# Performance work log

Measured on AMD Instinct MI355X. Metric: run time of the kernel, lower is better.

## Reference

```python
import jax, jax.numpy as jnp
import numpy as np

B, T, H, K, C, U, IN = 128, 800, 512, 10, 80, 64, 3


def setup_inputs() -> dict:
    key = jax.random.key(0)
    ks = jax.random.split(key, 6)
    s = 0.08  # small init so exp() window params stay stable
    return {
        "strokes": jax.random.normal(ks[0], (B, T, IN), jnp.float32),
        "sentences": jax.random.randint(ks[1], (B, U), 0, C),
        "sentences_mask": jnp.ones((B, U), jnp.float32),
        "W_ih": jax.random.normal(ks[2], (4 * H, IN + C), jnp.float32) * s,
        "W_hh": jax.random.normal(ks[3], (4 * H, H), jnp.float32) * s,
        "b_ih": jnp.zeros((4 * H,), jnp.float32),
        "b_hh": jnp.zeros((4 * H,), jnp.float32),
        "W_win": jax.random.normal(ks[4], (3 * K, H), jnp.float32) * s,
        "b_win": jnp.zeros((3 * K,), jnp.float32),
    }


def reference(strokes, sentences, sentences_mask, W_ih, W_hh, b_ih, b_hh, W_win, b_win):
    # Pre-mask the one-hot character encoding: [B, U, C]
    onehot = jax.nn.one_hot(sentences, C, dtype=jnp.float32) * sentences_mask[:, :, None]
    u = jnp.arange(U, dtype=jnp.float32)  # character position grid
    bias = b_ih + b_hh

    def step(carry, x_t):
        h, c, kappa_prev, window = carry
        inp = jnp.concatenate([x_t, window], axis=-1)           # [B, IN+C]
        gates = inp @ W_ih.T + h @ W_hh.T + bias                 # [B, 4H]
        i, f, g, o = jnp.split(gates, 4, axis=-1)                # torch LSTMCell order i,f,g,o
        i, f, o = jax.nn.sigmoid(i), jax.nn.sigmoid(f), jax.nn.sigmoid(o)
        c = f * c + i * jnp.tanh(g)
        h = o * jnp.tanh(c)
        # Gaussian window parameters (eq. 48-51 in Graves 2013)
        p = h @ W_win.T + b_win                                  # [B, 3K]
        a_hat, b_hat, k_hat = jnp.split(p, 3, axis=-1)
        alpha = jnp.exp(a_hat)
        beta = jnp.exp(b_hat)
        kappa = kappa_prev + jnp.exp(k_hat)
        # phi[b,u] = sum_k alpha * exp(-beta * (kappa - u)^2)
        d = kappa[:, :, None] - u[None, None, :]                 # [B, K, U]
        phi = jnp.sum(alpha[:, :, None] * jnp.exp(-beta[:, :, None] * d * d), axis=1)  # [B, U]
        window = jnp.einsum('bu,buc->bc', phi, onehot)           # [B, C]
        return (h, c, kappa, window), (h, window, phi)

    init = (
        jnp.zeros((B, H), jnp.float32),
        jnp.zeros((B, H), jnp.float32),
        jnp.zeros((B, K), jnp.float32),
        jnp.zeros((B, C), jnp.float32),
    )
    xs = jnp.swapaxes(strokes, 0, 1)                             # [T, B, IN]
    _, (h_seq, w_seq, phi_seq) = jax.lax.scan(step, init, xs)
    return (
        jnp.swapaxes(h_seq, 0, 1),    # [B, T, H]
        jnp.swapaxes(w_seq, 0, 1),    # [B, T, C]
        jnp.swapaxes(phi_seq, 0, 1),  # [B, T, U]
    )
```

## Files before the change

### kernel.cpp

```cpp
#include <hip/hip_runtime.h>
#include <hip/hip_bf16.h>
#include <math.h>

#define B_   128
#define T_   800
#define H_   512
#define K_   10
#define C_   80
#define U_   64
#define IN_  3
#define SDIM (H_ + C_)

#define NG   4
#define BPG  64
#define BT   32
#define UPB  8
#define RPB  32
#define NT   512

#define WS_ST    0
#define WS_GPP   (2*SDIM*B_)
#define WS_BAR   (WS_GPP + NG*BPG*BT*30)
#define WS_TOTAL (WS_BAR + NG*8*32)

#define OFF_H    0ull
#define OFF_W    ((size_t)B_ * T_ * H_)
#define OFF_PHI  (OFF_W + (size_t)B_ * T_ * C_)

__device__ __forceinline__ void st_bypass(float* p, float v) {
  asm volatile("global_store_dword %0, %1, off sc0 sc1" :: "v"(p), "v"(v) : "memory");
}
__device__ __forceinline__ void fence_vm() {
  asm volatile("s_waitcnt vmcnt(0)" ::: "memory");
}
__device__ __forceinline__ void flag_add(unsigned* p) {
  __hip_atomic_fetch_add(p, 1u, __ATOMIC_RELAXED, __HIP_MEMORY_SCOPE_AGENT);
}
__device__ __forceinline__ unsigned flag_sum(unsigned* base, int nlines) {
  unsigned s = 0;
  for (int i = 0; i < nlines; ++i)
    s += __hip_atomic_load(base + i * 32, __ATOMIC_RELAXED, __HIP_MEMORY_SCOPE_AGENT);
  return s;
}
__device__ __forceinline__ void acq_fence(unsigned* p) {
  (void)__hip_atomic_load(p, __ATOMIC_ACQUIRE, __HIP_MEMORY_SCOPE_AGENT);
}
__device__ __forceinline__ float sigmoidf_(float v) { return 1.0f / (1.0f + expf(-v)); }

__global__ void __launch_bounds__(256, 2)
init_ws_kernel(float* __restrict__ ws) {
  size_t i = (size_t)blockIdx.x * 256 + threadIdx.x;
  const size_t n = (size_t)WS_TOTAL;
  const size_t stride = (size_t)gridDim.x * 256;
  for (; i < n; i += stride) ws[i] = 0.0f;
}

__global__ void __launch_bounds__(NT, 1)
graves_kernel(const float* __restrict__ x,
              const int*   __restrict__ sent,
              const float* __restrict__ smask,
              const float* __restrict__ W_ih,
              const float* __restrict__ W_hh,
              const float* __restrict__ b_ih,
              const float* __restrict__ b_hh,
              const float* __restrict__ W_win,
              const float* __restrict__ b_win,
              float* __restrict__ out,
              float* __restrict__ ws)
{
  const int tid = threadIdx.x;
  const int bid = blockIdx.x;
  const int g   = bid / BPG;
  const int ub  = bid - g * BPG;
  const int b0  = g * BT;
  const int u0  = ub * UPB;

  float* sT  = ws + WS_ST;
  float* gpp = ws + WS_GPP;
  unsigned* fb = (unsigned*)(ws + WS_BAR) + (size_t)g * (8 * 32);
  unsigned* c1 = fb;
  unsigned* c2 = fb + 4 * 32;

  __shared__ __align__(16) float wlds[SDIM][RPB];
  __shared__ float red[NT][17];
  __shared__ float gl[RPB][BT];
  __shared__ float hT[UPB][BT];
  __shared__ float cpl[UPB][BT];
  __shared__ float wwin[UPB][30];
  __shared__ float xwb[RPB][4];
  __shared__ float ppst[BPG][30];
  __shared__ float pl[30];
  __shared__ float abk[3][K_];
  __shared__ float kapl[K_];
  __shared__ float phim[U_];
  __shared__ float phir[U_];
  __shared__ float wl[C_];
  __shared__ int   sentl[U_];
  __shared__ float maskl[U_];

  for (int idx = tid; idx < SDIM * RPB; idx += NT) {
    const int k = idx >> 5, r = idx & 31;
    const int uu = r >> 2, gate = r & 3;
    const int gr = gate * H_ + u0 + uu;
    wlds[k][r] = (k < H_) ? W_hh[(size_t)gr * H_ + k]
                          : W_ih[(size_t)gr * (IN_ + C_) + IN_ + (k - H_)];
  }
  if (tid < RPB) {
    const int uu = tid >> 2, gate = tid & 3, gr = gate * H_ + u0 + uu;
    xwb[tid][0] = W_ih[(size_t)gr * (IN_ + C_) + 0];
    xwb[tid][1] = W_ih[(size_t)gr * (IN_ + C_) + 1];
    xwb[tid][2] = W_ih[(size_t)gr * (IN_ + C_) + 2];
    xwb[tid][3] = b_ih[gr] + b_hh[gr];
  }
  if (tid < UPB * 30) {
    const int uu = tid / 30, j = tid % 30;
    wwin[uu][j] = W_win[(size_t)j * H_ + u0 + uu];
  }
  if (tid < UPB * BT) {
    cpl[tid >> 5][tid & 31] = 0.0f;
  }
  const bool isWB = (ub < BT);
  const int  wb_b = b0 + ub;
  if (isWB) {
    if (tid < U_) {
      sentl[tid] = sent[wb_b * U_ + tid];
      maskl[tid] = smask[wb_b * U_ + tid];
    }
    if (tid < K_) kapl[tid] = 0.0f;
  }
  __syncthreads();

  const int rt  = tid & 7;
  const int bt  = (tid >> 3) & 7;
  const int ks  = tid >> 6;
  const int myb = b0 + 4 * bt;

  for (int t = 0; t < T_; ++t) {
    const int p = t & 1;
    const float* sIn = sT + (size_t)p * (SDIM * B_);
    float*      sOut = sT + (size_t)(1 - p) * (SDIM * B_);

    float acc[4][4];
    #pragma unroll
    for (int i = 0; i < 4; ++i)
      #pragma unroll
      for (int j = 0; j < 4; ++j) acc[i][j] = 0.0f;

    {
      const float* sp = sIn + myb;
      const int k0 = ks * (H_ / 8);
      #pragma unroll 4
      for (int k = k0; k < k0 + H_ / 8; ++k) {
        const float4 s4 = *(const float4*)(sp + (size_t)k * B_);
        const float4 w4 = *(const float4*)(&wlds[k][4 * rt]);
        const float sv[4] = {s4.x, s4.y, s4.z, s4.w};
        const float wv[4] = {w4.x, w4.y, w4.z, w4.w};
        #pragma unroll
        for (int i = 0; i < 4; ++i)
          #pragma unroll
          for (int j = 0; j < 4; ++j) acc[i][j] = fmaf(wv[i], sv[j], acc[i][j]);
      }
    }

    if (tid == 0 && t > 0) {
      const unsigned tgt = (unsigned)(BT * t);
      while (flag_sum(c2, 2) < tgt) __builtin_amdgcn_s_sleep(1);
      acq_fence(c2);
    }
    __syncthreads();

    {
      const float* sp = sIn + myb;
      const int k0 = H_ + ks * (C_ / 8);
      #pragma unroll
      for (int k = k0; k < k0 + C_ / 8; ++k) {
        const float4 s4 = *(const float4*)(sp + (size_t)k * B_);
        const float4 w4 = *(const float4*)(&wlds[k][4 * rt]);
        const float sv[4] = {s4.x, s4.y, s4.z, s4.w};
        const float wv[4] = {w4.x, w4.y, w4.z, w4.w};
        #pragma unroll
        for (int i = 0; i < 4; ++i)
          #pragma unroll
          for (int j = 0; j < 4; ++j) acc[i][j] = fmaf(wv[i], sv[j], acc[i][j]);
      }
    }

    #pragma unroll
    for (int i = 0; i < 4; ++i)
      #pragma unroll
      for (int j = 0; j < 4; ++j) red[tid][i * 4 + j] = acc[i][j];
    __syncthreads();

    for (int it = tid; it < RPB * BT; it += NT) {
      const int r = it >> 5, b = it & 31;
      const int base = (r >> 2) + 8 * (b >> 2);
      const int e = (r & 3) * 4 + (b & 3);
      float v = xwb[r][3];
      #pragma unroll
      for (int kq = 0; kq < 8; ++kq) v += red[base + 64 * kq][e];
      const float* xp = x + ((size_t)(b0 + b) * T_ + t) * IN_;
      v = fmaf(xwb[r][0], xp[0], v);
      v = fmaf(xwb[r][1], xp[1], v);
      v = fmaf(xwb[r][2], xp[2], v);
      gl[r][b] = v;
    }
    __syncthreads();

    if (tid < BT * UPB) {
      const int b = tid & 31, uu = tid >> 5;
      const float iv = sigmoidf_(gl[uu * 4 + 0][b]);
      const float fv = sigmoidf_(gl[uu * 4 + 1][b]);
      const float gv = tanhf(gl[uu * 4 + 2][b]);
      const float ov = sigmoidf_(gl[uu * 4 + 3][b]);
      const float cv = fmaf(fv, cpl[uu][b], iv * gv);
      cpl[uu][b] = cv;
      const float hv = ov * tanhf(cv);
      hT[uu][b] = hv;
      st_bypass(&sOut[(size_t)(u0 + uu) * B_ + b0 + b], hv);
    }
    __syncthreads();

    for (int it = tid; it < BT * 30; it += NT) {
      const int b = it / 30, j = it % 30;
      float s = 0.0f;
      #pragma unroll
      for (int uu = 0; uu < UPB; ++uu) s = fmaf(wwin[uu][j], hT[uu][b], s);
      st_bypass(&gpp[((size_t)(g * BPG + ub) * BT + b) * 30 + j], s);
    }
    fence_vm();
    __syncthreads();
    if (tid == 0) flag_add(c1 + (ub & 3) * 32);

    if (!isWB) {
      if (tid < 64) {
        const int b = tid >> 1, half = tid & 1;
        float4 hv4 = make_float4(hT[half * 4 + 0][b], hT[half * 4 + 1][b],
                                 hT[half * 4 + 2][b], hT[half * 4 + 3][b]);
        *(float4*)&out[OFF_H + ((size_t)(b0 + b) * T_ + t) * H_ + u0 + half * 4] = hv4;
      }
      if (tid == 0) {
        const unsigned tgt = (unsigned)(BPG * (t + 1));
        while (flag_sum(c1, 4) < tgt) __builtin_amdgcn_s_sleep(1);
        acq_fence(c1);
      }
      __syncthreads();
    } else {
      if (tid == 0) {
        const unsigned tgt = (unsigned)(BPG * (t + 1));
        while (flag_sum(c1, 4) < tgt) __builtin_amdgcn_s_sleep(1);
        acq_fence(c1);
      }
      __syncthreads();
      for (int it = tid; it < BPG * 30; it += NT) {
        const int blk = it / 30, j = it % 30;
        ppst[blk][j] = gpp[((size_t)(g * BPG + blk) * BT + ub) * 30 + j];
      }
      __syncthreads();
      if (tid < 30) {
        float s = b_win[tid];
        #pragma unroll
        for (int blk = 0; blk < BPG; ++blk) s += ppst[blk][tid];
        pl[tid] = s;
      }
      __syncthreads();
      if (tid < K_) {
        abk[0][tid] = expf(pl[tid]);
        abk[1][tid] = expf(pl[K_ + tid]);
        const float kv = kapl[tid] + expf(pl[2 * K_ + tid]);
        kapl[tid] = kv;
        abk[2][tid] = kv;
      }
      __syncthreads();
      if (tid < U_) {
        const float fu = (float)tid;
        float s = 0.0f;
        #pragma unroll
        for (int j2 = 0; j2 < K_; ++j2) {
          const float d = abk[2][j2] - fu;
          s = fmaf(abk[0][j2], expf(-abk[1][j2] * d * d), s);
        }
        phim[tid] = s * maskl[tid];
        phir[tid] = s;
      }
      __syncthreads();
      if (tid < C_) {
        float wv = 0.0f;
        #pragma unroll
        for (int u = 0; u < U_; ++u) wv += (sentl[u] == tid) ? phim[u] : 0.0f;
        st_bypass(&sOut[(size_t)(H_ + tid) * B_ + wb_b], wv);
        wl[tid] = wv;
      }
      fence_vm();
      __syncthreads();
      if (tid == 0) flag_add(c2 + (ub & 1) * 32);

      if (tid < 64) {
        const int b = tid >> 1, half = tid & 1;
        float4 hv4 = make_float4(hT[half * 4 + 0][b], hT[half * 4 + 1][b],
                                 hT[half * 4 + 2][b], hT[half * 4 + 3][b]);
        *(float4*)&out[OFF_H + ((size_t)(b0 + b) * T_ + t) * H_ + u0 + half * 4] = hv4;
      }
      if (tid < U_) out[OFF_PHI + ((size_t)wb_b * T_ + t) * U_ + tid] = phir[tid];
      if (tid < C_) out[OFF_W + ((size_t)wb_b * T_ + t) * C_ + tid] = wl[tid];
    }
  }
}

extern "C" void kernel_launch(void* const* d_in, const int* in_sizes, int n_in,
                              void* d_out, int out_size, void* d_ws, size_t ws_size,
                              hipStream_t stream) {
  const float* x     = (const float*)d_in[0];
  const int*   sent  = (const int*)  d_in[1];
  const float* smask = (const float*)d_in[2];
  const float* W_ih  = (const float*)d_in[3];
  const float* W_hh  = (const float*)d_in[4];
  const float* b_ih  = (const float*)d_in[5];
  const float* b_hh  = (const float*)d_in[6];
  const float* W_win = (const float*)d_in[7];
  const float* b_win = (const float*)d_in[8];
  float* ws = (float*)d_ws;
  float* out = (float*)d_out;

  hipLaunchKernelGGL(init_ws_kernel, dim3(512), dim3(256), 0, stream, ws);
  hipLaunchKernelGGL(graves_kernel, dim3(NG * BPG), dim3(NT), 0, stream,
                     x, sent, smask, W_ih, W_hh, b_ih, b_hh, W_win, b_win, out, ws);
}
```

Measured before the change: 11.35 ms.

## Use split-bf16 MFMA for LSTM gate matmul and restructure step pipeline

Replaces the scalar FP32 FMA gate matmul with bf16 MFMA 16x16x32. Weights and state are split into hi and lo bf16 parts and combined over three MFMAs to keep near-FP32 accuracy. State is exchanged as packed hi/lo words in a row-major swizzled LDS layout, and threads per block drop to 256. The window computation is moved to the start of the next step so it can overlap with the h-part of the matmul. This cuts ALU cost, but adds per-step unpacking and changes the synchronisation ordering, and the split-bf16 approximation carries some precision risk.

After: 10.54 ms. 1.08x faster.

```diff
diff --git a/kernel.cpp b/kernel.cpp
--- a/kernel.cpp
+++ b/kernel.cpp
@@ -9,25 +9,32 @@
 #define C_   80
 #define U_   64
 #define IN_  3
-#define SDIM (H_ + C_)
 
 #define NG   4
 #define BPG  64
 #define BT   32
-#define UPB  8
-#define RPB  32
-#define NT   512
-
-#define WS_ST    0
-#define WS_GPP   (2*SDIM*B_)
-#define WS_BAR   (WS_GPP + NG*BPG*BT*30)
-#define WS_TOTAL (WS_BAR + NG*8*32)
+#define NT   256
+#define KROW 608
+
+#define WS_GPP_F (2*B_*KROW)
+#define WS_BAR_F (WS_GPP_F + NG*BPG*BT*30)
+#define WS_TOTAL_F (WS_BAR_F + NG*8*32)
 
 #define OFF_H    0ull
 #define OFF_W    ((size_t)B_ * T_ * H_)
 #define OFF_PHI  (OFF_W + (size_t)B_ * T_ * C_)
 
-__device__ __forceinline__ void st_bypass(float* p, float v) {
+typedef __attribute__((ext_vector_type(8))) short short8;
+typedef __attribute__((ext_vector_type(4))) float f32x4;
+
+#define SWZB(row)    (((row) ^ ((row) >> 2)) & 3)
+#define SWIDX(row,k) ((row)*KROW + ((((k) >> 3) ^ SWZB(row)) << 3) + ((k) & 7))
+#define LDFRAG(arr,row,u) (*(const short8*)&(arr)[(row)*KROW + (((u) ^ SWZB(row)) << 3)])
+
+__device__ __forceinline__ void stb_f32(float* p, float v) {
+  asm volatile("global_store_dword %0, %1, off sc0 sc1" :: "v"(p), "v"(v) : "memory");
+}
+__device__ __forceinline__ void stb_u32(unsigned* p, unsigned v) {
   asm volatile("global_store_dword %0, %1, off sc0 sc1" :: "v"(p), "v"(v) : "memory");
 }
 __device__ __forceinline__ void fence_vm() {
@@ -46,11 +53,17 @@
   (void)__hip_atomic_load(p, __ATOMIC_ACQUIRE, __HIP_MEMORY_SCOPE_AGENT);
 }
 __device__ __forceinline__ float sigmoidf_(float v) { return 1.0f / (1.0f + expf(-v)); }
+__device__ __forceinline__ unsigned pack_hl(float v) {
+  unsigned hb = __float_as_uint(v) >> 16;
+  float rs = v - __uint_as_float(hb << 16);
+  unsigned lb = __float_as_uint(rs) >> 16;
+  return (hb << 16) | lb;
+}
 
 __global__ void __launch_bounds__(256, 2)
 init_ws_kernel(float* __restrict__ ws) {
   size_t i = (size_t)blockIdx.x * 256 + threadIdx.x;
-  const size_t n = (size_t)WS_TOTAL;
+  const size_t n = (size_t)WS_TOTAL_F;
   const size_t stride = (size_t)gridDim.x * 256;
   for (; i < n; i += stride) ws[i] = 0.0f;
 }
@@ -70,205 +83,160 @@
 {
   const int tid = threadIdx.x;
   const int bid = blockIdx.x;
-  const int g   = bid / BPG;
-  const int ub  = bid - g * BPG;
+  const int g   = bid >> 6;
+  const int ub  = bid & (BPG - 1);
   const int b0  = g * BT;
-  const int u0  = ub * UPB;
-
-  float* sT  = ws + WS_ST;
-  float* gpp = ws + WS_GPP;
-  unsigned* fb = (unsigned*)(ws + WS_BAR) + (size_t)g * (8 * 32);
-  unsigned* c1 = fb;
-  unsigned* c2 = fb + 4 * 32;
-
-  __shared__ __align__(16) float wlds[SDIM][RPB];
-  __shared__ float red[NT][17];
-  __shared__ float gl[RPB][BT];
-  __shared__ float hT[UPB][BT];
-  __shared__ float cpl[UPB][BT];
-  __shared__ float wwin[UPB][30];
-  __shared__ float xwb[RPB][4];
-  __shared__ float ppst[BPG][30];
-  __shared__ float pl[30];
-  __shared__ float abk[3][K_];
-  __shared__ float kapl[K_];
-  __shared__ float phim[U_];
-  __shared__ float phir[U_];
-  __shared__ float wl[C_];
+  const int u0  = ub * 8;
+
+  unsigned* gbufu = (unsigned*)ws;
+  float*    gpp   = ws + WS_GPP_F;
+  unsigned* fb    = (unsigned*)(ws + WS_BAR_F) + (size_t)g * 256;
+  unsigned* c1l   = fb;
+  unsigned* c2l   = fb + 4 * 32;
+
+  __shared__ __align__(16) short whi[32 * KROW];
+  __shared__ __align__(16) short wlo[32 * KROW];
+  __shared__ __align__(16) short shi[32 * KROW];
+  __shared__ __align__(16) short slo[32 * KROW];
+  __shared__ __align__(16) float glf[1024];
+  __shared__ float hT[8 * 32];
+  __shared__ float wwin[8 * 30];
+  __shared__ float xwb[32 * 4];
   __shared__ int   sentl[U_];
   __shared__ float maskl[U_];
-
-  for (int idx = tid; idx < SDIM * RPB; idx += NT) {
-    const int k = idx >> 5, r = idx & 31;
-    const int uu = r >> 2, gate = r & 3;
-    const int gr = gate * H_ + u0 + uu;
-    wlds[k][r] = (k < H_) ? W_hh[(size_t)gr * H_ + k]
-                          : W_ih[(size_t)gr * (IN_ + C_) + IN_ + (k - H_)];
-  }
-  if (tid < RPB) {
+  __shared__ float kapl[K_ + 6];
+
+  float* pred  = glf;
+  float* pl    = glf + 256;
+  float* abkA  = glf + 288;
+  float* abkB  = glf + 304;
+  float* abkK  = glf + 320;
+  float* phim  = glf + 336;
+
+  for (int idx = tid; idx < 32 * KROW; idx += NT) {
+    const int r = idx / KROW, k = idx - r * KROW;
+    const int uu = r >> 2, gate = r & 3, gr = gate * H_ + u0 + uu;
+    float wv = 0.0f;
+    if (k < H_)      wv = W_hh[(size_t)gr * H_ + k];
+    else if (k < H_ + C_) wv = W_ih[(size_t)gr * (IN_ + C_) + IN_ + (k - H_)];
+    const unsigned hb = __float_as_uint(wv) >> 16;
+    const float rs = wv - __uint_as_float(hb << 16);
+    const unsigned lb = __float_as_uint(rs) >> 16;
+    const int li = SWIDX(r, k);
+    whi[li] = (short)hb;
+    wlo[li] = (short)lb;
+  }
+  for (int idx = tid; idx < 32 * 16; idx += NT) {
+    const int b2 = idx >> 4, k = (H_ + C_) + (idx & 15);
+    shi[SWIDX(b2, k)] = 0; slo[SWIDX(b2, k)] = 0;
+  }
+  if (tid < 32) {
     const int uu = tid >> 2, gate = tid & 3, gr = gate * H_ + u0 + uu;
-    xwb[tid][0] = W_ih[(size_t)gr * (IN_ + C_) + 0];
-    xwb[tid][1] = W_ih[(size_t)gr * (IN_ + C_) + 1];
-    xwb[tid][2] = W_ih[(size_t)gr * (IN_ + C_) + 2];
-    xwb[tid][3] = b_ih[gr] + b_hh[gr];
-  }
-  if (tid < UPB * 30) {
-    const int uu = tid / 30, j = tid % 30;
-    wwin[uu][j] = W_win[(size_t)j * H_ + u0 + uu];
-  }
-  if (tid < UPB * BT) {
-    cpl[tid >> 5][tid & 31] = 0.0f;
+    xwb[tid * 4 + 0] = W_ih[(size_t)gr * (IN_ + C_) + 0];
+    xwb[tid * 4 + 1] = W_ih[(size_t)gr * (IN_ + C_) + 1];
+    xwb[tid * 4 + 2] = W_ih[(size_t)gr * (IN_ + C_) + 2];
+    xwb[tid * 4 + 3] = b_ih[gr] + b_hh[gr];
+  }
+  for (int idx = tid; idx < 240; idx += NT) {
+    const int uu = idx / 30, j = idx - uu * 30;
+    wwin[idx] = W_win[(size_t)j * H_ + u0 + uu];
   }
   const bool isWB = (ub < BT);
   const int  wb_b = b0 + ub;
   if (isWB) {
-    if (tid < U_) {
-      sentl[tid] = sent[wb_b * U_ + tid];
-      maskl[tid] = smask[wb_b * U_ + tid];
-    }
+    if (tid < U_) { sentl[tid] = sent[wb_b * U_ + tid]; maskl[tid] = smask[wb_b * U_ + tid]; }
     if (tid < K_) kapl[tid] = 0.0f;
   }
   __syncthreads();
 
-  const int rt  = tid & 7;
-  const int bt  = (tid >> 3) & 7;
-  const int ks  = tid >> 6;
-  const int myb = b0 + 4 * bt;
-
-  for (int t = 0; t < T_; ++t) {
-    const int p = t & 1;
-    const float* sIn = sT + (size_t)p * (SDIM * B_);
-    float*      sOut = sT + (size_t)(1 - p) * (SDIM * B_);
-
-    float acc[4][4];
-    #pragma unroll
-    for (int i = 0; i < 4; ++i)
-      #pragma unroll
-      for (int j = 0; j < 4; ++j) acc[i][j] = 0.0f;
-
-    {
-      const float* sp = sIn + myb;
-      const int k0 = ks * (H_ / 8);
-      #pragma unroll 4
-      for (int k = k0; k < k0 + H_ / 8; ++k) {
-        const float4 s4 = *(const float4*)(sp + (size_t)k * B_);
-        const float4 w4 = *(const float4*)(&wlds[k][4 * rt]);
-        const float sv[4] = {s4.x, s4.y, s4.z, s4.w};
-        const float wv[4] = {w4.x, w4.y, w4.z, w4.w};
-        #pragma unroll
-        for (int i = 0; i < 4; ++i)
-          #pragma unroll
-          for (int j = 0; j < 4; ++j) acc[i][j] = fmaf(wv[i], sv[j], acc[i][j]);
-      }
-    }
+  const int lane = tid & 63;
+  const int wid  = tid >> 6;
+  const int ni   = wid & 1;
+  const int kh   = wid >> 1;
+  const int r16  = lane & 15;
+  const int g4   = lane >> 4;
+  const int bb   = ni * 16 + r16;
+
+  float cr0 = 0.0f, cr1 = 0.0f;
+
+#define GSTEP(ks) { \
+    const int uu_ = (ks) * 4 + g4; \
+    const short8 bh = LDFRAG(shi, bb, uu_); \
+    const short8 bl = LDFRAG(slo, bb, uu_); \
+    const short8 ah0 = LDFRAG(whi, r16, uu_); \
+    const short8 al0 = LDFRAG(wlo, r16, uu_); \
+    const short8 ah1 = LDFRAG(whi, 16 + r16, uu_); \
+    const short8 al1 = LDFRAG(wlo, 16 + r16, uu_); \
+    a0 = __builtin_amdgcn_mfma_f32_16x16x32_bf16(ah0, bh, a0, 0, 0, 0); \
+    a0 = __builtin_amdgcn_mfma_f32_16x16x32_bf16(ah0, bl, a0, 0, 0, 0); \
+    a0 = __builtin_amdgcn_mfma_f32_16x16x32_bf16(al0, bh, a0, 0, 0, 0); \
+    a1 = __builtin_amdgcn_mfma_f32_16x16x32_bf16(ah1, bh, a1, 0, 0, 0); \
+    a1 = __builtin_amdgcn_mfma_f32_16x16x32_bf16(ah1, bl, a1, 0, 0, 0); \
+    a1 = __builtin_amdgcn_mfma_f32_16x16x32_bf16(al1, bh, a1, 0, 0, 0); \
+  }
+
+  for (int t = 0; t <= T_; ++t) {
+    if (!isWB && t == T_) break;
+
+    const unsigned* pIn  = gbufu + (size_t)((t & 1) ^ 1) * (B_ * KROW);
+    unsigned*       pInW = gbufu + (size_t)((t & 1) ^ 1) * (B_ * KROW);
+    unsigned*       pOut = gbufu + (size_t)(t & 1) * (B_ * KROW);
 
     if (tid == 0 && t > 0) {
-      const unsigned tgt = (unsigned)(BT * t);
-      while (flag_sum(c2, 2) < tgt) __builtin_amdgcn_s_sleep(1);
-      acq_fence(c2);
-    }
-    __syncthreads();
-
-    {
-      const float* sp = sIn + myb;
-      const int k0 = H_ + ks * (C_ / 8);
-      #pragma unroll
-      for (int k = k0; k < k0 + C_ / 8; ++k) {
-        const float4 s4 = *(const float4*)(sp + (size_t)k * B_);
-        const float4 w4 = *(const float4*)(&wlds[k][4 * rt]);
-        const float sv[4] = {s4.x, s4.y, s4.z, s4.w};
-        const float wv[4] = {w4.x, w4.y, w4.z, w4.w};
-        #pragma unroll
-        for (int i = 0; i < 4; ++i)
-          #pragma unroll
-          for (int j = 0; j < 4; ++j) acc[i][j] = fmaf(wv[i], sv[j], acc[i][j]);
-      }
-    }
-
-    #pragma unroll
-    for (int i = 0; i < 4; ++i)
-      #pragma unroll
-      for (int j = 0; j < 4; ++j) red[tid][i * 4 + j] = acc[i][j];
-    __syncthreads();
-
-    for (int it = tid; it < RPB * BT; it += NT) {
-      const int r = it >> 5, b = it & 31;
-      const int base = (r >> 2) + 8 * (b >> 2);
-      const int e = (r & 3) * 4 + (b & 3);
-      float v = xwb[r][3];
-      #pragma unroll
-      for (int kq = 0; kq < 8; ++kq) v += red[base + 64 * kq][e];
-      const float* xp = x + ((size_t)(b0 + b) * T_ + t) * IN_;
-      v = fmaf(xwb[r][0], xp[0], v);
-      v = fmaf(xwb[r][1], xp[1], v);
-      v = fmaf(xwb[r][2], xp[2], v);
-      gl[r][b] = v;
-    }
-    __syncthreads();
-
-    if (tid < BT * UPB) {
-      const int b = tid & 31, uu = tid >> 5;
-      const float iv = sigmoidf_(gl[uu * 4 + 0][b]);
-      const float fv = sigmoidf_(gl[uu * 4 + 1][b]);
-      const float gv = tanhf(gl[uu * 4 + 2][b]);
-      const float ov = sigmoidf_(gl[uu * 4 + 3][b]);
-      const float cv = fmaf(fv, cpl[uu][b], iv * gv);
-      cpl[uu][b] = cv;
-      const float hv = ov * tanhf(cv);
-      hT[uu][b] = hv;
-      st_bypass(&sOut[(size_t)(u0 + uu) * B_ + b0 + b], hv);
-    }
-    __syncthreads();
-
-    for (int it = tid; it < BT * 30; it += NT) {
-      const int b = it / 30, j = it % 30;
-      float s = 0.0f;
-      #pragma unroll
-      for (int uu = 0; uu < UPB; ++uu) s = fmaf(wwin[uu][j], hT[uu][b], s);
-      st_bypass(&gpp[((size_t)(g * BPG + ub) * BT + b) * 30 + j], s);
-    }
-    fence_vm();
-    __syncthreads();
-    if (tid == 0) flag_add(c1 + (ub & 3) * 32);
-
-    if (!isWB) {
-      if (tid < 64) {
-        const int b = tid >> 1, half = tid & 1;
-        float4 hv4 = make_float4(hT[half * 4 + 0][b], hT[half * 4 + 1][b],
-                                 hT[half * 4 + 2][b], hT[half * 4 + 3][b]);
-        *(float4*)&out[OFF_H + ((size_t)(b0 + b) * T_ + t) * H_ + u0 + half * 4] = hv4;
-      }
-      if (tid == 0) {
-        const unsigned tgt = (unsigned)(BPG * (t + 1));
-        while (flag_sum(c1, 4) < tgt) __builtin_amdgcn_s_sleep(1);
-        acq_fence(c1);
-      }
-      __syncthreads();
-    } else {
-      if (tid == 0) {
-        const unsigned tgt = (unsigned)(BPG * (t + 1));
-        while (flag_sum(c1, 4) < tgt) __builtin_amdgcn_s_sleep(1);
-        acq_fence(c1);
-      }
-      __syncthreads();
-      for (int it = tid; it < BPG * 30; it += NT) {
-        const int blk = it / 30, j = it % 30;
-        ppst[blk][j] = gpp[((size_t)(g * BPG + blk) * BT + ub) * 30 + j];
-      }
+      const unsigned tgt = 64u * (unsigned)t;
+      while (flag_sum(c1l, 4) < tgt) __builtin_amdgcn_s_sleep(1);
+      acq_fence(c1l);
+    }
+    __syncthreads();
+
+    float xv0 = 0.f, xv1 = 0.f, xv2 = 0.f;
+    float pv0=0,pv1=0,pv2=0,pv3=0,pv4=0,pv5=0,pv6=0,pv7=0;
+    if (t < T_) {
+      const int sb = tid & 31, seg = tid >> 5;
+      const unsigned* grow = pIn + (size_t)(b0 + sb) * KROW + seg * 64;
+      uint4 v[16];
+      #pragma unroll
+      for (int i = 0; i < 16; ++i) v[i] = *(const uint4*)(grow + i * 4);
+      #pragma unroll
+      for (int i = 0; i < 16; ++i) {
+        const int k = seg * 64 + i * 4;
+        const int idx = SWIDX(sb, k);
+        const unsigned h01 = (v[i].x >> 16) | ((v[i].y >> 16) << 16);
+        const unsigned h23 = (v[i].z >> 16) | ((v[i].w >> 16) << 16);
+        const unsigned l01 = (v[i].x & 0xffffu) | ((v[i].y & 0xffffu) << 16);
+        const unsigned l23 = (v[i].z & 0xffffu) | ((v[i].w & 0xffffu) << 16);
+        *(uint2*)&shi[idx] = make_uint2(h01, h23);
+        *(uint2*)&slo[idx] = make_uint2(l01, l23);
+      }
+      if (kh == 0) {
+        const float* xp = x + ((size_t)(b0 + bb) * T_ + t) * IN_;
+        xv0 = xp[0]; xv1 = xp[1]; xv2 = xp[2];
+      }
+    }
+    if (isWB && t >= 1 && tid < 240) {
+      const int j = tid % 30, ch = tid / 30;
+      const float* gp = gpp + (((size_t)(g * BPG + ch * 8) * BT + ub) * 30 + j);
+      pv0 = gp[0*BT*30]; pv1 = gp[1*BT*30]; pv2 = gp[2*BT*30]; pv3 = gp[3*BT*30];
+      pv4 = gp[4*BT*30]; pv5 = gp[5*BT*30]; pv6 = gp[6*BT*30]; pv7 = gp[7*BT*30];
+    }
+    __syncthreads();
+
+    if (isWB && t >= 1) {
+      if (tid < 240) pred[tid] = ((pv0+pv1)+(pv2+pv3))+((pv4+pv5)+(pv6+pv7));
       __syncthreads();
       if (tid < 30) {
         float s = b_win[tid];
         #pragma unroll
-        for (int blk = 0; blk < BPG; ++blk) s += ppst[blk][tid];
+        for (int ch = 0; ch < 8; ++ch) s += pred[ch * 30 + tid];
         pl[tid] = s;
       }
       __syncthreads();
       if (tid < K_) {
-        abk[0][tid] = expf(pl[tid]);
-        abk[1][tid] = expf(pl[K_ + tid]);
+        abkA[tid] = expf(pl[tid]);
+        abkB[tid] = expf(pl[K_ + tid]);
         const float kv = kapl[tid] + expf(pl[2 * K_ + tid]);
         kapl[tid] = kv;
-        abk[2][tid] = kv;
+        abkK[tid] = kv;
       }
       __syncthreads();
       if (tid < U_) {
@@ -276,34 +244,98 @@
         float s = 0.0f;
         #pragma unroll
         for (int j2 = 0; j2 < K_; ++j2) {
-          const float d = abk[2][j2] - fu;
-          s = fmaf(abk[0][j2], expf(-abk[1][j2] * d * d), s);
+          const float d = abkK[j2] - fu;
+          s = fmaf(abkA[j2], expf(-abkB[j2] * d * d), s);
         }
         phim[tid] = s * maskl[tid];
-        phir[tid] = s;
+        out[OFF_PHI + ((size_t)wb_b * T_ + (t - 1)) * U_ + tid] = s;
       }
       __syncthreads();
       if (tid < C_) {
         float wv = 0.0f;
         #pragma unroll
         for (int u = 0; u < U_; ++u) wv += (sentl[u] == tid) ? phim[u] : 0.0f;
-        st_bypass(&sOut[(size_t)(H_ + tid) * B_ + wb_b], wv);
-        wl[tid] = wv;
+        stb_u32(&pInW[(size_t)wb_b * KROW + H_ + tid], pack_hl(wv));
+        out[OFF_W + ((size_t)wb_b * T_ + (t - 1)) * C_ + tid] = wv;
       }
       fence_vm();
       __syncthreads();
-      if (tid == 0) flag_add(c2 + (ub & 1) * 32);
-
-      if (tid < 64) {
-        const int b = tid >> 1, half = tid & 1;
-        float4 hv4 = make_float4(hT[half * 4 + 0][b], hT[half * 4 + 1][b],
-                                 hT[half * 4 + 2][b], hT[half * 4 + 3][b]);
-        *(float4*)&out[OFF_H + ((size_t)(b0 + b) * T_ + t) * H_ + u0 + half * 4] = hv4;
-      }
-      if (tid < U_) out[OFF_PHI + ((size_t)wb_b * T_ + t) * U_ + tid] = phir[tid];
-      if (tid < C_) out[OFF_W + ((size_t)wb_b * T_ + t) * C_ + tid] = wl[tid];
-    }
-  }
+      if (tid == 0) flag_add(c2l + (ub & 1) * 32);
+    }
+    if (t == T_) break;
+
+    f32x4 a0 = {0.f, 0.f, 0.f, 0.f}, a1 = {0.f, 0.f, 0.f, 0.f};
+    for (int ks = kh * 8; ks < kh * 8 + 8; ++ks) GSTEP(ks);
+
+    if (tid == 0 && t > 0) {
+      const unsigned tgt = 32u * (unsigned)t;
+      while (flag_sum(c2l, 2) < tgt) __builtin_amdgcn_s_sleep(1);
+      acq_fence(c2l);
+    }
+    __syncthreads();
+
+    {
+      const int sb = tid & 31, seg = tid >> 5;
+      #pragma unroll
+      for (int i = 0; i < 10; ++i) {
+        const int c = seg * 10 + i;
+        const unsigned v = pIn[(size_t)(b0 + sb) * KROW + H_ + c];
+        const int idx = SWIDX(sb, H_ + c);
+        shi[idx] = (short)(v >> 16);
+        slo[idx] = (short)(v & 0xffffu);
+      }
+    }
+    __syncthreads();
+
+    if (kh == 0) { GSTEP(16); }
+    else         { GSTEP(17); GSTEP(18); }
+
+    if (kh == 1) {
+      #pragma unroll
+      for (int e = 0; e < 4; ++e) {
+        glf[(ni * 2 + 0) * 256 + (g4 * 4 + e) * 16 + r16] = a0[e];
+        glf[(ni * 2 + 1) * 256 + (g4 * 4 + e) * 16 + r16] = a1[e];
+      }
+    }
+    __syncthreads();
+    if (kh == 0) {
+      #pragma unroll
+      for (int mi = 0; mi < 2; ++mi) {
+        float ge[4];
+        #pragma unroll
+        for (int e = 0; e < 4; ++e) {
+          const int r = mi * 16 + g4 * 4 + e;
+          const float av = ((mi == 0) ? a0[e] : a1[e]) + glf[(ni * 2 + mi) * 256 + (g4 * 4 + e) * 16 + r16];
+          ge[e] = av + xwb[r*4+0]*xv0 + xwb[r*4+1]*xv1 + xwb[r*4+2]*xv2 + xwb[r*4+3];
+        }
+        const float iv = sigmoidf_(ge[0]);
+        const float fv = sigmoidf_(ge[1]);
+        const float gv = tanhf(ge[2]);
+        const float ov = sigmoidf_(ge[3]);
+        const float cprev = (mi == 0) ? cr0 : cr1;
+        const float cv = fmaf(fv, cprev, iv * gv);
+        if (mi == 0) cr0 = cv; else cr1 = cv;
+        const float hv = ov * tanhf(cv);
+        const int uu = mi * 4 + g4;
+        hT[uu * 32 + bb] = hv;
+        stb_u32(&pOut[(size_t)(b0 + bb) * KROW + (u0 + uu)], pack_hl(hv));
+        out[OFF_H + ((size_t)(b0 + bb) * T_ + t) * H_ + (u0 + uu)] = hv;
+      }
+    }
+    __syncthreads();
+
+    for (int it = tid; it < BT * 30; it += NT) {
+      const int b2 = it / 30, j = it - b2 * 30;
+      float s = 0.0f;
+      #pragma unroll
+      for (int uu = 0; uu < 8; ++uu) s = fmaf(wwin[uu * 30 + j], hT[uu * 32 + b2], s);
+      stb_f32(&gpp[((size_t)bid * BT + b2) * 30 + j], s);
+    }
+    fence_vm();
+    __syncthreads();
+    if (tid == 0) flag_add(c1l + (ub & 3) * 32);
+  }
+#undef GSTEP
 }
 
 extern "C" void kernel_launch(void* const* d_in, const int* in_sizes, int n_in,
@@ -318,7 +350,7 @@
   const float* b_hh  = (const float*)d_in[6];
   const float* W_win = (const float*)d_in[7];
   const float* b_win = (const float*)d_in[8];
-  float* ws = (float*)d_ws;
+  float* ws  = (float*)d_ws;
   float* out = (float*)d_out;
 
   hipLaunchKernelGGL(init_ws_kernel, dim3(512), dim3(256), 0, stream, ws);
```
